# Optimization experiments

Measured on AMD Instinct MI355X. Metric: run time of the kernel, lower is better.

## Reference

```python
import jax, jax.numpy as jnp
import numpy as np

B, N, L, C, H = 2, 3000, 6, 128, 1
IN_DIM = 6
SIGMA_D = 1.0
EPS = 1e-5
DH = C // H


def _conv1(x, W, b):
    # pointwise Conv1d: x [B,Cin,N], W [Cout,Cin], b [Cout]
    return jnp.einsum('oc,bcn->bon', W, x) + b[None, :, None]


def _bn(x, g, beta):
    # BatchNorm1d (training-mode batch stats) over (B, N) per channel
    m = x.mean(axis=(0, 2), keepdims=True)
    v = x.var(axis=(0, 2), keepdims=True)
    return g[None, :, None] * (x - m) * jax.lax.rsqrt(v + EPS) + beta[None, :, None]


def setup_inputs() -> dict:
    key = jax.random.key(0)
    ks = iter(jax.random.split(key, 80))

    def w(shape, fan_in):
        return jax.random.normal(next(ks), shape, jnp.float32) * (1.0 / np.sqrt(fan_in))

    src = jax.random.normal(next(ks), (B, N, 3), jnp.float32)
    tgt = src + 0.1 * jax.random.normal(next(ks), (B, N, 3), jnp.float32)
    corr_pos = jnp.concatenate([src, tgt], axis=-1)  # [B,N,6]

    d = {
        'corr_pos': corr_pos, 'src_keypts': src, 'tgt_keypts': tgt,
        'init_W': w((C, IN_DIM), IN_DIM), 'init_b': jnp.zeros((C,), jnp.float32),
        'pcn_W': w((L, C, C), C), 'pcn_b': jnp.zeros((L, C), jnp.float32),
        'pcn_g': jnp.ones((L, C), jnp.float32), 'pcn_beta': jnp.zeros((L, C), jnp.float32),
        'qW': w((L, C, C), C), 'qb': jnp.zeros((L, C), jnp.float32),
        'kW': w((L, C, C), C), 'kb': jnp.zeros((L, C), jnp.float32),
        'vW': w((L, C, C), C), 'vb': jnp.zeros((L, C), jnp.float32),
        'm1W': w((L, C // 2, C), C), 'm1b': jnp.zeros((L, C // 2), jnp.float32),
        'm1g': jnp.ones((L, C // 2), jnp.float32), 'm1beta': jnp.zeros((L, C // 2), jnp.float32),
        'm2W': w((L, C // 2, C // 2), C // 2), 'm2b': jnp.zeros((L, C // 2), jnp.float32),
        'm2g': jnp.ones((L, C // 2), jnp.float32), 'm2beta': jnp.zeros((L, C // 2), jnp.float32),
        'm3W': w((L, C, C // 2), C // 2), 'm3b': jnp.zeros((L, C), jnp.float32),
        'c1W': w((32, C), C), 'c1b': jnp.zeros((32,), jnp.float32),
        'c2W': w((32, 32), 32), 'c2b': jnp.zeros((32,), jnp.float32),
        'c3W': w((1, 32), 32), 'c3b': jnp.zeros((1,), jnp.float32),
    }
    return d


def reference(corr_pos, src_keypts, tgt_keypts, init_W, init_b,
              pcn_W, pcn_b, pcn_g, pcn_beta,
              qW, qb, kW, kb, vW, vb,
              m1W, m1b, m1g, m1beta, m2W, m2b, m2g, m2beta, m3W, m3b,
              c1W, c1b, c2W, c2b, c3W, c3b):
    # spatial compatibility: clamp(1 - (d_src - d_tgt)^2 / sigma_d^2, min=0)  [B,N,N]
    src_dist = jnp.linalg.norm(src_keypts[:, :, None, :] - src_keypts[:, None, :, :], axis=-1)
    tgt_dist = jnp.linalg.norm(tgt_keypts[:, :, None, :] - tgt_keypts[:, None, :, :], axis=-1)
    sc = jnp.maximum(1.0 - (src_dist - tgt_dist) ** 2 / SIGMA_D ** 2, 0.0)

    # init embedding: [B,C,N]
    x = _conv1(jnp.swapaxes(corr_pos, 1, 2), init_W, init_b)
    scale = 1.0 / jnp.sqrt(jnp.float32(DH))

    for i in range(L):
        # PointCN layer
        x = jax.nn.relu(_bn(_conv1(x, pcn_W[i], pcn_b[i]), pcn_g[i], pcn_beta[i]))
        # NonLocal block
        Q = _conv1(x, qW[i], qb[i]).reshape(B, H, DH, N)
        K = _conv1(x, kW[i], kb[i]).reshape(B, H, DH, N)
        V = _conv1(x, vW[i], vb[i]).reshape(B, H, DH, N)
        scores = jnp.einsum('bhco,bhci->bhoi', Q, K) * scale  # [B,H,N,N]
        weight = jax.nn.softmax(sc[:, None, :, :] * scores, axis=-1)
        msg = jnp.einsum('bhoi,bhci->bhco', weight, V).reshape(B, C, N)
        msg = jax.nn.relu(_bn(_conv1(msg, m1W[i], m1b[i]), m1g[i], m1beta[i]))
        msg = jax.nn.relu(_bn(_conv1(msg, m2W[i], m2b[i]), m2g[i], m2beta[i]))
        msg = _conv1(msg, m3W[i], m3b[i])
        x = x + msg

    corr_feat = x
    norm = jnp.maximum(jnp.linalg.norm(corr_feat, axis=1, keepdims=True), 1e-12)
    normed_corr_feat = corr_feat / norm
    h = jax.nn.relu(_conv1(corr_feat, c1W, c1b))
    h = jax.nn.relu(_conv1(h, c2W, c2b))
    confidence = _conv1(h, c3W, c3b)[:, 0, :]  # [B,N]
    return confidence, normed_corr_feat
```

## Files before the change

kernel.cpp:

```cpp
#include <hip/hip_runtime.h>
#include <hip/hip_bf16.h>


#define BB 2
#define NN 3000
#define CC 128
#define LAYERS 6
#define BN_EPS 1e-5f
#define ATT_SCALE 0.08838834764831845f
#define INV_CNT (1.f / (float)(BB * NN))

typedef _Float16 f16;
typedef _Float16 f16x8 __attribute__((ext_vector_type(8)));
typedef float f32x4 __attribute__((ext_vector_type(4)));

__global__ void init_conv(const float* __restrict__ corr, const float* __restrict__ W,
                          const float* __restrict__ bias, float* __restrict__ x) {
  int idx = blockIdx.x * 256 + threadIdx.x;
  if (idx >= BB * CC * NN) return;
  int n = idx % NN;
  int c = (idx / NN) % CC;
  int b = idx / (NN * CC);
  const float* cp = corr + (b * NN + n) * 6;
  float acc = bias[c];
#pragma unroll
  for (int d = 0; d < 6; ++d) acc += W[c * 6 + d] * cp[d];
  x[idx] = acc;
}

template <int CIN, int COUT, int NP, int MODE, int CSPLIT, int BNIN, int STATS>
__launch_bounds__(256)
__global__ void conv_k(const float* __restrict__ in, float* __restrict__ out,
                       const float* __restrict__ W, const float* __restrict__ bias,
                       const float* __restrict__ res,
                       const float* __restrict__ isums, const float* __restrict__ ig,
                       const float* __restrict__ ibeta,
                       const float* __restrict__ rsums, const float* __restrict__ rg,
                       const float* __restrict__ rbeta, float* __restrict__ osums) {
  constexpr int COB = COUT / CSPLIT;
  constexpr int CH = (CIN > 64) ? 64 : CIN;
  constexpr int PG = NP / 4;
  constexpr int KPT = COB * PG / 256;
  constexpr int XROW = (NP == 16) ? 20 : 32;
  __shared__ alignas(16) float Xs[CIN][XROW];
  __shared__ float Ws[COB][CH + 1];
  __shared__ float bnsc[BNIN ? CIN : 1], bnsh[BNIN ? CIN : 1];
  const int tid = threadIdx.x;
  const int p0 = blockIdx.x * NP;
  const int co0 = blockIdx.y * COB;

  if (BNIN) {
    for (int c = tid; c < CIN; c += 256) {
      float s = isums[c], s2 = isums[CIN + c];
      float mean = s * INV_CNT;
      float var = s2 * INV_CNT - mean * mean;
      float sc = ig[c] * rsqrtf(var + BN_EPS);
      bnsc[c] = sc;
      bnsh[c] = ibeta[c] - mean * sc;
    }
    __syncthreads();
  }

  for (int idx = tid; idx < CIN * NP; idx += 256) {
    int ci = idx / NP, j = idx % NP;
    int p = p0 + j;
    float v = 0.f;
    if (p < BB * NN) {
      int b = p / NN, n = p % NN;
      v = in[(b * CIN + ci) * NN + n];
      if (BNIN) {
        v = v * bnsc[ci] + bnsh[ci];
        v = v > 0.f ? v : 0.f;
      }
    }
    Xs[ci][j] = v;
  }

  const int nb = (tid % PG) * 4;
  const int cb = (tid / PG) * KPT;

  float acc[KPT][4];
#pragma unroll
  for (int k = 0; k < KPT; ++k)
#pragma unroll
    for (int j = 0; j < 4; ++j) acc[k][j] = 0.f;

  for (int c0 = 0; c0 < CIN; c0 += CH) {
    __syncthreads();
    for (int idx = tid; idx < COB * CH; idx += 256) {
      int co = idx / CH, cc = idx % CH;
      Ws[co][cc] = W[(co0 + co) * CIN + c0 + cc];
    }
    __syncthreads();
#pragma unroll 4
    for (int cc = 0; cc < CH; ++cc) {
      float4 xv = *reinterpret_cast<const float4*>(&Xs[c0 + cc][nb]);
#pragma unroll
      for (int k = 0; k < KPT; ++k) {
        float w = Ws[cb + k][cc];
        acc[k][0] += w * xv.x;
        acc[k][1] += w * xv.y;
        acc[k][2] += w * xv.z;
        acc[k][3] += w * xv.w;
      }
    }
  }

#pragma unroll
  for (int k = 0; k < KPT; ++k) {
    int co = co0 + cb + k;
    float bv = bias[co];
    float rsc = 0.f, rsh = 0.f;
    if (MODE == 3) {
      float s = rsums[co], s2 = rsums[COUT + co];
      float mean = s * INV_CNT;
      float var = s2 * INV_CNT - mean * mean;
      rsc = rg[co] * rsqrtf(var + BN_EPS);
      rsh = rbeta[co] - mean * rsc;
    }
    float sp = 0.f, sp2 = 0.f;
#pragma unroll
    for (int j = 0; j < 4; ++j) {
      int p = p0 + nb + j;
      if (p < BB * NN) {
        int b = p / NN, n = p % NN;
        int o = (b * COUT + co) * NN + n;
        float v = acc[k][j] + bv;
        if (MODE == 3) {
          float rr = res[o] * rsc + rsh;
          v += (rr > 0.f ? rr : 0.f);
        }
        out[o] = v;
        if (STATS) {
          sp += v;
          sp2 += v * v;
        }
      }
    }
    if (STATS) {
#pragma unroll
      for (int d = 1; d < PG; d <<= 1) {
        sp += __shfl_xor(sp, d);
        sp2 += __shfl_xor(sp2, d);
      }
      if ((tid & (PG - 1)) == 0) {
        atomicAdd(&osums[co], sp);
        atomicAdd(&osums[COUT + co], sp2);
      }
    }
  }
}

__launch_bounds__(256)
__global__ void conv_qkv(const float* __restrict__ Yp, const float* __restrict__ psums,
                         const float* __restrict__ pg, const float* __restrict__ pbeta,
                         const float* __restrict__ qW, const float* __restrict__ kW,
                         const float* __restrict__ vW, const float* __restrict__ qb,
                         const float* __restrict__ kb, const float* __restrict__ vb,
                         f16* __restrict__ Qh, f16* __restrict__ Ql,
                         f16* __restrict__ Kh, f16* __restrict__ Kl,
                         f16* __restrict__ Vh, f16* __restrict__ Vl) {
  __shared__ alignas(16) float Xs[128][32];
  __shared__ float Ws[64][65];
  __shared__ float bnsc[128], bnsh[128];
  const int tid = threadIdx.x;
  const int p0 = blockIdx.x * 32;
  const int sel = blockIdx.y >> 1;
  const int co0 = (blockIdx.y & 1) * 64;
  const float* W = (sel == 0) ? qW : (sel == 1) ? kW : vW;
  const float* bias = (sel == 0) ? qb : (sel == 1) ? kb : vb;

  for (int c = tid; c < 128; c += 256) {
    float s = psums[c], s2 = psums[128 + c];
    float mean = s * INV_CNT;
    float var = s2 * INV_CNT - mean * mean;
    float sc = pg[c] * rsqrtf(var + BN_EPS);
    bnsc[c] = sc;
    bnsh[c] = pbeta[c] - mean * sc;
  }
  __syncthreads();

  for (int idx = tid; idx < 128 * 32; idx += 256) {
    int ci = idx >> 5, j = idx & 31;
    int p = p0 + j;
    float v = 0.f;
    if (p < BB * NN) {
      int b = p / NN, n = p % NN;
      v = Yp[(b * 128 + ci) * NN + n];
      v = v * bnsc[ci] + bnsh[ci];
      v = v > 0.f ? v : 0.f;
    }
    Xs[ci][j] = v;
  }

  const int nb = (tid % 8) * 4;
  const int cb = (tid / 8) * 2;
  float acc[2][4] = {{0.f, 0.f, 0.f, 0.f}, {0.f, 0.f, 0.f, 0.f}};

  for (int c0 = 0; c0 < 128; c0 += 64) {
    __syncthreads();
    for (int idx = tid; idx < 64 * 64; idx += 256) {
      int co = idx >> 6, cc = idx & 63;
      Ws[co][cc] = W[(co0 + co) * 128 + c0 + cc];
    }
    __syncthreads();
#pragma unroll 4
    for (int cc = 0; cc < 64; ++cc) {
      float4 xv = *reinterpret_cast<const float4*>(&Xs[c0 + cc][nb]);
#pragma unroll
      for (int k = 0; k < 2; ++k) {
        float w = Ws[cb + k][cc];
        acc[k][0] += w * xv.x;
        acc[k][1] += w * xv.y;
        acc[k][2] += w * xv.z;
        acc[k][3] += w * xv.w;
      }
    }
  }

#pragma unroll
  for (int k = 0; k < 2; ++k) {
    int co = co0 + cb + k;
    float bv = bias[co];
#pragma unroll
    for (int j = 0; j < 4; ++j) {
      int p = p0 + nb + j;
      if (p < BB * NN) {
        int b = p / NN, n = p % NN;
        float v = acc[k][j] + bv;
        f16 h = (f16)v;
        f16 lo = (f16)(v - (float)h);
        if (sel == 0) {
          size_t o = (size_t)(b * NN + n) * CC + co;
          Qh[o] = h; Ql[o] = lo;
        } else if (sel == 1) {
          size_t o = (size_t)(b * NN + n) * CC + co;
          Kh[o] = h; Kl[o] = lo;
        } else {
          size_t o = (size_t)(b * CC + co) * NN + n;
          Vh[o] = h; Vl[o] = lo;
        }
      }
    }
  }
}

__launch_bounds__(512)
__global__ void attn_mf7(const f16* __restrict__ Qhp, const f16* __restrict__ Qlp,
                         const f16* __restrict__ Khp, const f16* __restrict__ Klp,
                         const f16* __restrict__ Vhp, const f16* __restrict__ Vlp,
                         const float* __restrict__ srcp, const float* __restrict__ tgtp,
                         float* __restrict__ pacc, float* __restrict__ pm,
                         float* __restrict__ pl, int chunk) {
  const int b = blockIdx.z;
  const int q0 = blockIdx.x * 128;
  const int s = blockIdx.y;
  const int cs = s * chunk;
  const int ce = min(cs + chunk, NN);
  const int tid = threadIdx.x;
  const int w = tid >> 6, lane = tid & 63, quad = lane >> 4, l15 = lane & 15;

  __shared__ f16 Ksh[32][136], Ksl[32][136];
  __shared__ f16 Vsh[128][40], Vsl[128][40];
  __shared__ f16 Ps[8][16][40];
  __shared__ float kps[6][36];

  float qp[4][6];
  const int orow = q0 + w * 16;
#pragma unroll
  for (int r = 0; r < 4; ++r) {
    int o = orow + quad * 4 + r;
    if (o >= NN) o = NN - 1;
#pragma unroll
    for (int d = 0; d < 3; ++d) {
      qp[r][d] = srcp[(b * NN + o) * 3 + d];
      qp[r][3 + d] = tgtp[(b * NN + o) * 3 + d];
    }
  }
  f16x8 qh[4], ql[4];
  {
    int o = orow + l15;
    if (o >= NN) o = NN - 1;
    size_t base = (size_t)(b * NN + o) * CC + quad * 8;
#pragma unroll
    for (int cc = 0; cc < 4; ++cc) {
      qh[cc] = *reinterpret_cast<const f16x8*>(Qhp + base + cc * 32);
      ql[cc] = *reinterpret_cast<const f16x8*>(Qlp + base + cc * 32);
    }
  }

  float m[4], l[4];
#pragma unroll
  for (int r = 0; r < 4; ++r) {
    m[r] = -1e30f;
    l[r] = 0.f;
  }
  f32x4 acco[8];
#pragma unroll
  for (int t = 0; t < 8; ++t) acco[t] = (f32x4){0.f, 0.f, 0.f, 0.f};

  const int NT = (ce - cs + 31) >> 5;
  for (int it = 0; it < NT; ++it) {
    const int kk0 = cs + it * 32;
    __syncthreads();
    for (int t = tid; t < 1024; t += 512) {
      int plane = t >> 9, row = (t >> 4) & 31, cu = t & 15;
      int kr = kk0 + row;
      if (kr >= NN) kr = NN - 1;
      const f16* src = (plane ? Klp : Khp) + (size_t)(b * NN + kr) * CC + cu * 8;
      uint4 v = *reinterpret_cast<const uint4*>(src);
      f16* dst = plane ? &Ksl[row][cu * 8] : &Ksh[row][cu * 8];
      *reinterpret_cast<uint4*>(dst) = v;
    }
    for (int t = tid; t < 1024; t += 512) {
      int plane = t >> 9, c = (t >> 2) & 127, iu = t & 3;
      int kb = kk0 + iu * 8;
      if (kb > NN - 8) kb = NN - 8;
      const f16* src = (plane ? Vlp : Vhp) + (size_t)(b * CC + c) * NN + kb;
      uint4 v = *reinterpret_cast<const uint4*>(src);
      f16* dst = plane ? &Vsl[c][iu * 8] : &Vsh[c][iu * 8];
      *reinterpret_cast<uint4*>(dst) = v;
    }
    if (tid < 192) {
      int d = tid >> 5, i = tid & 31;
      int ig = kk0 + i;
      if (ig >= NN) ig = NN - 1;
      kps[d][i] = (d < 3) ? srcp[(b * NN + ig) * 3 + d] : tgtp[(b * NN + ig) * 3 + d - 3];
    }
    __syncthreads();

    f32x4 accs[2];
#pragma unroll
    for (int k4 = 0; k4 < 2; ++k4) accs[k4] = (f32x4){0.f, 0.f, 0.f, 0.f};
#pragma unroll
    for (int cc = 0; cc < 4; ++cc) {
#pragma unroll
      for (int k4 = 0; k4 < 2; ++k4) {
        f16x8 bh = *reinterpret_cast<const f16x8*>(&Ksh[k4 * 16 + l15][cc * 32 + quad * 8]);
        f16x8 bl = *reinterpret_cast<const f16x8*>(&Ksl[k4 * 16 + l15][cc * 32 + quad * 8]);
        accs[k4] = __builtin_amdgcn_mfma_f32_16x16x32_f16(qh[cc], bl, accs[k4], 0, 0, 0);
        accs[k4] = __builtin_amdgcn_mfma_f32_16x16x32_f16(ql[cc], bh, accs[k4], 0, 0, 0);
        accs[k4] = __builtin_amdgcn_mfma_f32_16x16x32_f16(qh[cc], bh, accs[k4], 0, 0, 0);
      }
    }

    float sv[2][4];
#pragma unroll
    for (int k4 = 0; k4 < 2; ++k4) {
      int iloc = k4 * 16 + l15;
      int ig = kk0 + iloc;
      float kx = kps[0][iloc], ky = kps[1][iloc], kz = kps[2][iloc];
      float tx = kps[3][iloc], ty = kps[4][iloc], tz = kps[5][iloc];
#pragma unroll
      for (int r = 0; r < 4; ++r) {
        float dx = qp[r][0] - kx, dy = qp[r][1] - ky, dz = qp[r][2] - kz;
        float ds2 = dx * dx + dy * dy + dz * dz;
        float ex = qp[r][3] - tx, ey = qp[r][4] - ty, ez = qp[r][5] - tz;
        float dt2 = ex * ex + ey * ey + ez * ez;
        float d2 = ds2 + dt2 - 2.f * sqrtf(ds2 * dt2);
        float gg = 1.f - d2;
        gg = gg > 0.f ? gg : 0.f;
        float val = accs[k4][r] * (ATT_SCALE * gg);
        sv[k4][r] = (ig < ce) ? val : -1e30f;
      }
    }

    float tmax[4];
#pragma unroll
    for (int r = 0; r < 4; ++r) tmax[r] = fmaxf(sv[0][r], sv[1][r]);
#pragma unroll
    for (int d = 1; d <= 8; d <<= 1)
#pragma unroll
      for (int r = 0; r < 4; ++r) tmax[r] = fmaxf(tmax[r], __shfl_xor(tmax[r], d));

    float alpha[4], ps[4];
    f16 pf[2][4];
#pragma unroll
    for (int r = 0; r < 4; ++r) {
      float mn = fmaxf(m[r], tmax[r]);
      alpha[r] = __expf(m[r] - mn);
      m[r] = mn;
      pf[0][r] = (f16)__expf(sv[0][r] - mn);
      pf[1][r] = (f16)__expf(sv[1][r] - mn);
      ps[r] = (float)pf[0][r] + (float)pf[1][r];
    }
#pragma unroll
    for (int d = 1; d <= 8; d <<= 1)
#pragma unroll
      for (int r = 0; r < 4; ++r) ps[r] += __shfl_xor(ps[r], d);
#pragma unroll
    for (int r = 0; r < 4; ++r) {
      l[r] = l[r] * alpha[r] + ps[r];
#pragma unroll
      for (int t = 0; t < 8; ++t) acco[t][r] *= alpha[r];
    }
#pragma unroll
    for (int r = 0; r < 4; ++r) {
      Ps[w][quad * 4 + r][l15] = pf[0][r];
      Ps[w][quad * 4 + r][16 + l15] = pf[1][r];
    }
    __syncthreads();

    {
      f16x8 af = *reinterpret_cast<const f16x8*>(&Ps[w][l15][quad * 8]);
#pragma unroll
      for (int t = 0; t < 8; ++t) {
        f16x8 vh = *reinterpret_cast<const f16x8*>(&Vsh[t * 16 + l15][quad * 8]);
        f16x8 vl = *reinterpret_cast<const f16x8*>(&Vsl[t * 16 + l15][quad * 8]);
        acco[t] = __builtin_amdgcn_mfma_f32_16x16x32_f16(af, vl, acco[t], 0, 0, 0);
        acco[t] = __builtin_amdgcn_mfma_f32_16x16x32_f16(af, vh, acco[t], 0, 0, 0);
      }
    }
  }

  const int pidx = s * BB + b;
  if (l15 == 0) {
#pragma unroll
    for (int r = 0; r < 4; ++r) {
      int o = orow + quad * 4 + r;
      if (o < NN) {
        pm[pidx * NN + o] = m[r];
        pl[pidx * NN + o] = l[r];
      }
    }
  }
#pragma unroll
  for (int r = 0; r < 4; ++r) {
    int o = orow + quad * 4 + r;
    if (o < NN) {
      size_t base2 = ((size_t)pidx * NN + o) * CC;
#pragma unroll
      for (int t = 0; t < 8; ++t) pacc[base2 + t * 16 + l15] = acco[t][r];
    }
  }
}

__launch_bounds__(256)
__global__ void conv_m1(const float* __restrict__ pacc, const float* __restrict__ pm,
                        const float* __restrict__ pl, float* __restrict__ out,
                        const float* __restrict__ W, const float* __restrict__ bias,
                        float* __restrict__ osums, int ksplit) {
  __shared__ alignas(16) float Xs[128][20];
  __shared__ float Ws[64][65];
  __shared__ float Es[16][17];
  __shared__ float Li[16];
  const int tid = threadIdx.x;
  const int p0 = blockIdx.x * 16;

  if (tid < 16) {
    int p = p0 + tid;
    float Lv = 1.f;
    if (p < BB * NN) {
      int b = p / NN, o = p % NN;
      float M = -1e30f;
      for (int s = 0; s < ksplit; ++s) M = fmaxf(M, pm[(s * BB + b) * NN + o]);
      Lv = 0.f;
      for (int s = 0; s < ksplit; ++s) {
        int pi = s * BB + b;
        float e = __expf(pm[pi * NN + o] - M);
        Es[tid][s] = e;
        Lv += pl[pi * NN + o] * e;
      }
    } else {
      for (int s = 0; s < ksplit; ++s) Es[tid][s] = 0.f;
    }
    Li[tid] = 1.f / Lv;
  }
  __syncthreads();

  for (int idx = tid; idx < 512; idx += 256) {
    int j = idx >> 5, c4 = (idx & 31) * 4;
    int p = p0 + j;
    float4 a = {0.f, 0.f, 0.f, 0.f};
    if (p < BB * NN) {
      int b = p / NN, o = p % NN;
      for (int s = 0; s < ksplit; ++s) {
        float e = Es[j][s];
        const float4 pv = *reinterpret_cast<const float4*>(
            &pacc[((size_t)(s * BB + b) * NN + o) * CC + c4]);
        a.x += pv.x * e;
        a.y += pv.y * e;
        a.z += pv.z * e;
        a.w += pv.w * e;
      }
      float inv = Li[j];
      a.x *= inv; a.y *= inv; a.z *= inv; a.w *= inv;
    }
    Xs[c4][j] = a.x;
    Xs[c4 + 1][j] = a.y;
    Xs[c4 + 2][j] = a.z;
    Xs[c4 + 3][j] = a.w;
  }

  const int nb = (tid & 3) * 4;
  const int co = tid >> 2;
  float acc[4] = {0.f, 0.f, 0.f, 0.f};

  for (int c0 = 0; c0 < 128; c0 += 64) {
    __syncthreads();
    for (int idx = tid; idx < 64 * 64; idx += 256) {
      int cr = idx >> 6, cc = idx & 63;
      Ws[cr][cc] = W[cr * 128 + c0 + cc];
    }
    __syncthreads();
#pragma unroll 4
    for (int cc = 0; cc < 64; ++cc) {
      float4 xv = *reinterpret_cast<const float4*>(&Xs[c0 + cc][nb]);
      float w = Ws[co][cc];
      acc[0] += w * xv.x;
      acc[1] += w * xv.y;
      acc[2] += w * xv.z;
      acc[3] += w * xv.w;
    }
  }

  {
    float bv = bias[co];
    float sp = 0.f, sp2 = 0.f;
#pragma unroll
    for (int j = 0; j < 4; ++j) {
      int p = p0 + nb + j;
      if (p < BB * NN) {
        int b = p / NN, n = p % NN;
        float v = acc[j] + bv;
        out[(b * 64 + co) * NN + n] = v;
        sp += v;
        sp2 += v * v;
      }
    }
    sp += __shfl_xor(sp, 1);
    sp2 += __shfl_xor(sp2, 1);
    sp += __shfl_xor(sp, 2);
    sp2 += __shfl_xor(sp2, 2);
    if ((tid & 3) == 0) {
      atomicAdd(&osums[co], sp);
      atomicAdd(&osums[64 + co], sp2);
    }
  }
}

__launch_bounds__(256)
__global__ void head_all(const float* __restrict__ Xg,
                         const float* __restrict__ c1W, const float* __restrict__ c1b,
                         const float* __restrict__ c2W, const float* __restrict__ c2b,
                         const float* __restrict__ c3W, const float* __restrict__ c3b,
                         float* __restrict__ out) {
  __shared__ float Xs[128][33];
  __shared__ float W1[32][129];
  __shared__ float W2[32][33];
  __shared__ float Hs[32][33], H2s[32][33];
  __shared__ float Inv[32];
  const int tid = threadIdx.x;
  const int p0 = blockIdx.x * 32;
  const int j = tid >> 3, sub = tid & 7;

  for (int idx = tid; idx < 128 * 32; idx += 256) {
    int ci = idx >> 5, jj = idx & 31;
    int p = p0 + jj;
    float v = 0.f;
    if (p < BB * NN) {
      int b = p / NN, n = p % NN;
      v = Xg[(b * 128 + ci) * NN + n];
    }
    Xs[ci][jj] = v;
  }
  for (int idx = tid; idx < 32 * 128; idx += 256) {
    W1[idx >> 7][idx & 127] = c1W[idx];
  }
  for (int idx = tid; idx < 32 * 32; idx += 256) {
    W2[idx >> 5][idx & 31] = c2W[idx];
  }
  __syncthreads();

  {
    float h1v[4];
#pragma unroll
    for (int k = 0; k < 4; ++k) h1v[k] = c1b[sub * 4 + k];
    for (int ci = 0; ci < 128; ++ci) {
      float xv = Xs[ci][j];
#pragma unroll
      for (int k = 0; k < 4; ++k) h1v[k] += W1[sub * 4 + k][ci] * xv;
    }
#pragma unroll
    for (int k = 0; k < 4; ++k) Hs[j][sub * 4 + k] = h1v[k] > 0.f ? h1v[k] : 0.f;
  }
  __syncthreads();
  {
    float h2v[4];
#pragma unroll
    for (int k = 0; k < 4; ++k) h2v[k] = c2b[sub * 4 + k];
#pragma unroll
    for (int cc = 0; cc < 32; ++cc) {
      float hv = Hs[j][cc];
#pragma unroll
      for (int k = 0; k < 4; ++k) h2v[k] += W2[sub * 4 + k][cc] * hv;
    }
#pragma unroll
    for (int k = 0; k < 4; ++k) H2s[j][sub * 4 + k] = h2v[k] > 0.f ? h2v[k] : 0.f;
  }
  __syncthreads();

  float ssp = 0.f;
#pragma unroll
  for (int k = 0; k < 16; ++k) {
    float v = Xs[sub + 8 * k][j];
    ssp += v * v;
  }
  ssp += __shfl_xor(ssp, 1);
  ssp += __shfl_xor(ssp, 2);
  ssp += __shfl_xor(ssp, 4);

  if (sub == 0) {
    int p = p0 + j;
    if (p < BB * NN) {
      float conf = c3b[0];
#pragma unroll
      for (int c = 0; c < 32; ++c) conf += c3W[c] * H2s[j][c];
      out[p] = conf;
    }
    float nrm = sqrtf(ssp);
    nrm = nrm > 1e-12f ? nrm : 1e-12f;
    Inv[j] = 1.f / nrm;
  }
  __syncthreads();

  for (int idx = tid; idx < 128 * 32; idx += 256) {
    int c = idx >> 5, jj = idx & 31;
    int p = p0 + jj;
    if (p < BB * NN) {
      int b = p / NN, n = p % NN;
      out[BB * NN + (b * 128 + c) * NN + n] = Xs[c][jj] * Inv[jj];
    }
  }
}

extern "C" void kernel_launch(void* const* d_in, const int* in_sizes, int n_in,
                              void* d_out, int out_size, void* d_ws, size_t ws_size,
                              hipStream_t stream) {
  const float* corr = (const float*)d_in[0];
  const float* srcp = (const float*)d_in[1];
  const float* tgtp = (const float*)d_in[2];
  const float* initW = (const float*)d_in[3];
  const float* initb = (const float*)d_in[4];
  const float* pcnW = (const float*)d_in[5];
  const float* pcnb = (const float*)d_in[6];
  const float* pcng = (const float*)d_in[7];
  const float* pcnbeta = (const float*)d_in[8];
  const float* qW = (const float*)d_in[9];
  const float* qb = (const float*)d_in[10];
  const float* kW = (const float*)d_in[11];
  const float* kb = (const float*)d_in[12];
  const float* vW = (const float*)d_in[13];
  const float* vb = (const float*)d_in[14];
  const float* m1W = (const float*)d_in[15];
  const float* m1b = (const float*)d_in[16];
  const float* m1g = (const float*)d_in[17];
  const float* m1beta = (const float*)d_in[18];
  const float* m2W = (const float*)d_in[19];
  const float* m2b = (const float*)d_in[20];
  const float* m2g = (const float*)d_in[21];
  const float* m2beta = (const float*)d_in[22];
  const float* m3W = (const float*)d_in[23];
  const float* m3b = (const float*)d_in[24];
  const float* c1W = (const float*)d_in[25];
  const float* c1b = (const float*)d_in[26];
  const float* c2W = (const float*)d_in[27];
  const float* c2b = (const float*)d_in[28];
  const float* c3W = (const float*)d_in[29];
  const float* c3b = (const float*)d_in[30];

  const int FEAT = BB * CC * NN;
  const int PLANE = FEAT / 2;
  float* ws = (float*)d_ws;
  float* X = ws;
  float* Y = X + FEAT;
  float* QhF = Y + FEAT;
  float* QlF = QhF + PLANE;
  float* KhF = QlF + PLANE;
  float* KlF = KhF + PLANE;
  float* VhF = KlF + PLANE;
  float* VlF = VhF + PLANE;
  float* SB = VlF + PLANE;
  float* pacc = SB + 3072;
  f16* Qh = (f16*)QhF;
  f16* Ql = (f16*)QlF;
  f16* Kh = (f16*)KhF;
  f16* Kl = (f16*)KlF;
  f16* Vh = (f16*)VhF;
  f16* Vl = (f16*)VlF;
  float* T1 = QhF;
  float* T2 = KhF;

  const size_t base_f = (size_t)(2 * FEAT + 6 * PLANE + 3072);
  const size_t per_f = (size_t)BB * NN * CC + 2 * (size_t)BB * NN;
  int ksplit = 16;
  while (ksplit > 1 && (base_f + (size_t)ksplit * per_f) * 4 > ws_size) ksplit >>= 1;
  const int chunk = (((NN + ksplit - 1) / ksplit) + 7) & ~7;
  float* pm = pacc + (size_t)ksplit * BB * NN * CC;
  float* pl = pm + (size_t)ksplit * BB * NN;

  dim3 blk(256);
  const int PT32 = (BB * NN + 31) / 32;
  const int PT16 = (BB * NN + 15) / 16;
  const int G_FEAT = (FEAT + 255) / 256;

  hipMemsetAsync(SB, 0, 3072 * sizeof(float), stream);
  init_conv<<<G_FEAT, blk, 0, stream>>>(corr, initW, initb, X);

  for (int i = 0; i < LAYERS; ++i) {
    float* pcnS = SB + i * 512;
    float* m1S = pcnS + 256;
    float* m2S = m1S + 128;
    conv_k<128, 128, 16, 0, 2, 0, 1><<<dim3(PT16, 2), blk, 0, stream>>>(
        X, Y, pcnW + i * 16384, pcnb + i * 128, nullptr,
        nullptr, nullptr, nullptr, nullptr, nullptr, nullptr, pcnS);
    conv_qkv<<<dim3(PT32, 6), blk, 0, stream>>>(
        Y, pcnS, pcng + i * 128, pcnbeta + i * 128, qW + i * 16384, kW + i * 16384,
        vW + i * 16384, qb + i * 128, kb + i * 128, vb + i * 128,
        Qh, Ql, Kh, Kl, Vh, Vl);
    attn_mf7<<<dim3((NN + 127) / 128, ksplit, BB), dim3(512), 0, stream>>>(
        Qh, Ql, Kh, Kl, Vh, Vl, srcp, tgtp, pacc, pm, pl, chunk);
    conv_m1<<<PT16, blk, 0, stream>>>(pacc, pm, pl, T1, m1W + i * 8192, m1b + i * 64,
                                      m1S, ksplit);
    conv_k<64, 64, 16, 0, 1, 1, 1><<<dim3(PT16, 1), blk, 0, stream>>>(
        T1, T2, m2W + i * 4096, m2b + i * 64, nullptr,
        m1S, m1g + i * 64, m1beta + i * 64, nullptr, nullptr, nullptr, m2S);
    conv_k<64, 128, 16, 3, 2, 1, 0><<<dim3(PT16, 2), blk, 0, stream>>>(
        T2, X, m3W + i * 8192, m3b + i * 128, Y,
        m2S, m2g + i * 64, m2beta + i * 64, pcnS, pcng + i * 128, pcnbeta + i * 128,
        nullptr);
  }

  head_all<<<PT32, blk, 0, stream>>>(X, c1W, c1b, c2W, c2b, c3W, c3b, (float*)d_out);
}
```

Measured before the change: 1.356 ms.

## Use split-fp16 MFMA for PointCN and QKV pointwise convolutions

Replaces the scalar FP32 FMA kernels for the PointCN conv and the fused Q/K/V projection with MFMA-based kernels. Inputs and weights are split into high and low fp16 halves, and three 16x16x32 MFMAs per tile approximate FP32 accuracy. Each block now covers all 128 output channels (one wave per 32 channels), which halves the number of grid slices and removes the repeated input loads. This costs extra conversion work and precision only near FP32, while the attention kernel likely still dominates total time.

```diff
diff --git a/kernel.cpp b/kernel.cpp
--- a/kernel.cpp
+++ b/kernel.cpp
@@ -26,6 +26,230 @@
 #pragma unroll
   for (int d = 0; d < 6; ++d) acc += W[c * 6 + d] * cp[d];
   x[idx] = acc;
+}
+
+__launch_bounds__(256)
+__global__ void conv_mfma_pcn(const float* __restrict__ Xg, float* __restrict__ Y,
+                              const float* __restrict__ W, const float* __restrict__ bias,
+                              float* __restrict__ osums) {
+  __shared__ f16 Xsh[32][136], Xsl[32][136];
+  __shared__ f16 Wsh[128][40], Wsl[128][40];
+  const int tid = threadIdx.x;
+  const int p0 = blockIdx.x * 32;
+  const int w = tid >> 6, lane = tid & 63, quad = lane >> 4, l15 = lane & 15;
+  const int co0 = w * 32;
+
+  for (int idx = tid; idx < 512; idx += 256) {
+    int ci = (idx >> 5) * 8, j = idx & 31;
+    int p = p0 + j;
+    if (p >= BB * NN) p = BB * NN - 1;
+    int b = p / NN, n = p % NN;
+    f16x8 hv, lv;
+#pragma unroll
+    for (int t = 0; t < 8; ++t) {
+      float v = Xg[(b * 128 + ci + t) * NN + n];
+      f16 h = (f16)v;
+      hv[t] = h;
+      lv[t] = (f16)(v - (float)h);
+    }
+    *reinterpret_cast<f16x8*>(&Xsh[j][ci]) = hv;
+    *reinterpret_cast<f16x8*>(&Xsl[j][ci]) = lv;
+  }
+
+  f32x4 acc[2][2];
+#pragma unroll
+  for (int ct = 0; ct < 2; ++ct)
+#pragma unroll
+    for (int pt = 0; pt < 2; ++pt) acc[ct][pt] = (f32x4){0.f, 0.f, 0.f, 0.f};
+
+  for (int kc = 0; kc < 4; ++kc) {
+    __syncthreads();
+    for (int idx = tid; idx < 512; idx += 256) {
+      int co = idx >> 2, ks = idx & 3;
+      const float* wp = W + co * 128 + kc * 32 + ks * 8;
+      float4 w0 = *reinterpret_cast<const float4*>(wp);
+      float4 w1 = *reinterpret_cast<const float4*>(wp + 4);
+      float wv[8] = {w0.x, w0.y, w0.z, w0.w, w1.x, w1.y, w1.z, w1.w};
+      f16x8 hv, lv;
+#pragma unroll
+      for (int t = 0; t < 8; ++t) {
+        f16 h = (f16)wv[t];
+        hv[t] = h;
+        lv[t] = (f16)(wv[t] - (float)h);
+      }
+      *reinterpret_cast<f16x8*>(&Wsh[co][ks * 8]) = hv;
+      *reinterpret_cast<f16x8*>(&Wsl[co][ks * 8]) = lv;
+    }
+    __syncthreads();
+#pragma unroll
+    for (int ct = 0; ct < 2; ++ct) {
+      f16x8 ah = *reinterpret_cast<const f16x8*>(&Wsh[co0 + ct * 16 + l15][quad * 8]);
+      f16x8 al = *reinterpret_cast<const f16x8*>(&Wsl[co0 + ct * 16 + l15][quad * 8]);
+#pragma unroll
+      for (int pt = 0; pt < 2; ++pt) {
+        f16x8 bh = *reinterpret_cast<const f16x8*>(&Xsh[pt * 16 + l15][kc * 32 + quad * 8]);
+        f16x8 bl = *reinterpret_cast<const f16x8*>(&Xsl[pt * 16 + l15][kc * 32 + quad * 8]);
+        acc[ct][pt] = __builtin_amdgcn_mfma_f32_16x16x32_f16(ah, bl, acc[ct][pt], 0, 0, 0);
+        acc[ct][pt] = __builtin_amdgcn_mfma_f32_16x16x32_f16(al, bh, acc[ct][pt], 0, 0, 0);
+        acc[ct][pt] = __builtin_amdgcn_mfma_f32_16x16x32_f16(ah, bh, acc[ct][pt], 0, 0, 0);
+      }
+    }
+  }
+
+  float sp[2][4] = {{0.f}}, sp2[2][4] = {{0.f}};
+#pragma unroll
+  for (int ct = 0; ct < 2; ++ct)
+#pragma unroll
+    for (int pt = 0; pt < 2; ++pt) {
+      int p = p0 + pt * 16 + l15;
+      if (p < BB * NN) {
+        int b = p / NN, n = p % NN;
+#pragma unroll
+        for (int r = 0; r < 4; ++r) {
+          int co = co0 + ct * 16 + quad * 4 + r;
+          float v = acc[ct][pt][r] + bias[co];
+          Y[(b * 128 + co) * NN + n] = v;
+          sp[ct][r] += v;
+          sp2[ct][r] += v * v;
+        }
+      }
+    }
+#pragma unroll
+  for (int ct = 0; ct < 2; ++ct)
+#pragma unroll
+    for (int r = 0; r < 4; ++r)
+#pragma unroll
+      for (int d = 1; d <= 8; d <<= 1) {
+        sp[ct][r] += __shfl_xor(sp[ct][r], d);
+        sp2[ct][r] += __shfl_xor(sp2[ct][r], d);
+      }
+  if (l15 == 0) {
+#pragma unroll
+    for (int ct = 0; ct < 2; ++ct)
+#pragma unroll
+      for (int r = 0; r < 4; ++r) {
+        int co = co0 + ct * 16 + quad * 4 + r;
+        atomicAdd(&osums[co], sp[ct][r]);
+        atomicAdd(&osums[128 + co], sp2[ct][r]);
+      }
+  }
+}
+
+__launch_bounds__(256)
+__global__ void conv_mfma_qkv(const float* __restrict__ Yp, const float* __restrict__ psums,
+                              const float* __restrict__ pg, const float* __restrict__ pbeta,
+                              const float* __restrict__ qW, const float* __restrict__ kW,
+                              const float* __restrict__ vW, const float* __restrict__ qb,
+                              const float* __restrict__ kb, const float* __restrict__ vb,
+                              f16* __restrict__ Qh, f16* __restrict__ Ql,
+                              f16* __restrict__ Kh, f16* __restrict__ Kl,
+                              f16* __restrict__ Vh, f16* __restrict__ Vl) {
+  __shared__ f16 Xsh[32][136], Xsl[32][136];
+  __shared__ f16 Wsh[128][40], Wsl[128][40];
+  __shared__ float bnsc[128], bnsh[128];
+  const int tid = threadIdx.x;
+  const int p0 = blockIdx.x * 32;
+  const int sel = blockIdx.y;
+  const int w = tid >> 6, lane = tid & 63, quad = lane >> 4, l15 = lane & 15;
+  const int co0 = w * 32;
+  const float* W = (sel == 0) ? qW : (sel == 1) ? kW : vW;
+  const float* bias = (sel == 0) ? qb : (sel == 1) ? kb : vb;
+
+  for (int c = tid; c < 128; c += 256) {
+    float s = psums[c], s2 = psums[128 + c];
+    float mean = s * INV_CNT;
+    float var = s2 * INV_CNT - mean * mean;
+    float sc = pg[c] * rsqrtf(var + BN_EPS);
+    bnsc[c] = sc;
+    bnsh[c] = pbeta[c] - mean * sc;
+  }
+  __syncthreads();
+
+  for (int idx = tid; idx < 512; idx += 256) {
+    int ci = (idx >> 5) * 8, j = idx & 31;
+    int p = p0 + j;
+    if (p >= BB * NN) p = BB * NN - 1;
+    int b = p / NN, n = p % NN;
+    f16x8 hv, lv;
+#pragma unroll
+    for (int t = 0; t < 8; ++t) {
+      float v = Yp[(b * 128 + ci + t) * NN + n];
+      v = v * bnsc[ci + t] + bnsh[ci + t];
+      v = v > 0.f ? v : 0.f;
+      f16 h = (f16)v;
+      hv[t] = h;
+      lv[t] = (f16)(v - (float)h);
+    }
+    *reinterpret_cast<f16x8*>(&Xsh[j][ci]) = hv;
+    *reinterpret_cast<f16x8*>(&Xsl[j][ci]) = lv;
+  }
+
+  f32x4 acc[2][2];
+#pragma unroll
+  for (int ct = 0; ct < 2; ++ct)
+#pragma unroll
+    for (int pt = 0; pt < 2; ++pt) acc[ct][pt] = (f32x4){0.f, 0.f, 0.f, 0.f};
+
+  for (int kc = 0; kc < 4; ++kc) {
+    __syncthreads();
+    for (int idx = tid; idx < 512; idx += 256) {
+      int co = idx >> 2, ks = idx & 3;
+      const float* wp = W + co * 128 + kc * 32 + ks * 8;
+      float4 w0 = *reinterpret_cast<const float4*>(wp);
+      float4 w1 = *reinterpret_cast<const float4*>(wp + 4);
+      float wv[8] = {w0.x, w0.y, w0.z, w0.w, w1.x, w1.y, w1.z, w1.w};
+      f16x8 hv, lv;
+#pragma unroll
+      for (int t = 0; t < 8; ++t) {
+        f16 h = (f16)wv[t];
+        hv[t] = h;
+        lv[t] = (f16)(wv[t] - (float)h);
+      }
+      *reinterpret_cast<f16x8*>(&Wsh[co][ks * 8]) = hv;
+      *reinterpret_cast<f16x8*>(&Wsl[co][ks * 8]) = lv;
+    }
+    __syncthreads();
+#pragma unroll
+    for (int ct = 0; ct < 2; ++ct) {
+      f16x8 ah = *reinterpret_cast<const f16x8*>(&Wsh[co0 + ct * 16 + l15][quad * 8]);
+      f16x8 al = *reinterpret_cast<const f16x8*>(&Wsl[co0 + ct * 16 + l15][quad * 8]);
+#pragma unroll
+      for (int pt = 0; pt < 2; ++pt) {
+        f16x8 bh = *reinterpret_cast<const f16x8*>(&Xsh[pt * 16 + l15][kc * 32 + quad * 8]);
+        f16x8 bl = *reinterpret_cast<const f16x8*>(&Xsl[pt * 16 + l15][kc * 32 + quad * 8]);
+        acc[ct][pt] = __builtin_amdgcn_mfma_f32_16x16x32_f16(ah, bl, acc[ct][pt], 0, 0, 0);
+        acc[ct][pt] = __builtin_amdgcn_mfma_f32_16x16x32_f16(al, bh, acc[ct][pt], 0, 0, 0);
+        acc[ct][pt] = __builtin_amdgcn_mfma_f32_16x16x32_f16(ah, bh, acc[ct][pt], 0, 0, 0);
+      }
+    }
+  }
+
+#pragma unroll
+  for (int ct = 0; ct < 2; ++ct)
+#pragma unroll
+    for (int pt = 0; pt < 2; ++pt) {
+      int p = p0 + pt * 16 + l15;
+      if (p < BB * NN) {
+        int b = p / NN, n = p % NN;
+#pragma unroll
+        for (int r = 0; r < 4; ++r) {
+          int co = co0 + ct * 16 + quad * 4 + r;
+          float v = acc[ct][pt][r] + bias[co];
+          f16 h = (f16)v;
+          f16 lo = (f16)(v - (float)h);
+          if (sel == 0) {
+            size_t o = (size_t)(b * NN + n) * CC + co;
+            Qh[o] = h; Ql[o] = lo;
+          } else if (sel == 1) {
+            size_t o = (size_t)(b * NN + n) * CC + co;
+            Kh[o] = h; Kl[o] = lo;
+          } else {
+            size_t o = (size_t)(b * CC + co) * NN + n;
+            Vh[o] = h; Vl[o] = lo;
+          }
+        }
+      }
+    }
 }
 
 template <int CIN, int COUT, int NP, int MODE, int CSPLIT, int BNIN, int STATS>
@@ -146,100 +370,6 @@
       if ((tid & (PG - 1)) == 0) {
         atomicAdd(&osums[co], sp);
         atomicAdd(&osums[COUT + co], sp2);
-      }
-    }
-  }
-}
-
-__launch_bounds__(256)
-__global__ void conv_qkv(const float* __restrict__ Yp, const float* __restrict__ psums,
-                         const float* __restrict__ pg, const float* __restrict__ pbeta,
-                         const float* __restrict__ qW, const float* __restrict__ kW,
-                         const float* __restrict__ vW, const float* __restrict__ qb,
-                         const float* __restrict__ kb, const float* __restrict__ vb,
-                         f16* __restrict__ Qh, f16* __restrict__ Ql,
-                         f16* __restrict__ Kh, f16* __restrict__ Kl,
-                         f16* __restrict__ Vh, f16* __restrict__ Vl) {
-  __shared__ alignas(16) float Xs[128][32];
-  __shared__ float Ws[64][65];
-  __shared__ float bnsc[128], bnsh[128];
-  const int tid = threadIdx.x;
-  const int p0 = blockIdx.x * 32;
-  const int sel = blockIdx.y >> 1;
-  const int co0 = (blockIdx.y & 1) * 64;
-  const float* W = (sel == 0) ? qW : (sel == 1) ? kW : vW;
-  const float* bias = (sel == 0) ? qb : (sel == 1) ? kb : vb;
-
-  for (int c = tid; c < 128; c += 256) {
-    float s = psums[c], s2 = psums[128 + c];
-    float mean = s * INV_CNT;
-    float var = s2 * INV_CNT - mean * mean;
-    float sc = pg[c] * rsqrtf(var + BN_EPS);
-    bnsc[c] = sc;
-    bnsh[c] = pbeta[c] - mean * sc;
-  }
-  __syncthreads();
-
-  for (int idx = tid; idx < 128 * 32; idx += 256) {
-    int ci = idx >> 5, j = idx & 31;
-    int p = p0 + j;
-    float v = 0.f;
-    if (p < BB * NN) {
-      int b = p / NN, n = p % NN;
-      v = Yp[(b * 128 + ci) * NN + n];
-      v = v * bnsc[ci] + bnsh[ci];
-      v = v > 0.f ? v : 0.f;
-    }
-    Xs[ci][j] = v;
-  }
-
-  const int nb = (tid % 8) * 4;
-  const int cb = (tid / 8) * 2;
-  float acc[2][4] = {{0.f, 0.f, 0.f, 0.f}, {0.f, 0.f, 0.f, 0.f}};
-
-  for (int c0 = 0; c0 < 128; c0 += 64) {
-    __syncthreads();
-    for (int idx = tid; idx < 64 * 64; idx += 256) {
-      int co = idx >> 6, cc = idx & 63;
-      Ws[co][cc] = W[(co0 + co) * 128 + c0 + cc];
-    }
-    __syncthreads();
-#pragma unroll 4
-    for (int cc = 0; cc < 64; ++cc) {
-      float4 xv = *reinterpret_cast<const float4*>(&Xs[c0 + cc][nb]);
-#pragma unroll
-      for (int k = 0; k < 2; ++k) {
-        float w = Ws[cb + k][cc];
-        acc[k][0] += w * xv.x;
-        acc[k][1] += w * xv.y;
-        acc[k][2] += w * xv.z;
-        acc[k][3] += w * xv.w;
-      }
-    }
-  }
-
-#pragma unroll
-  for (int k = 0; k < 2; ++k) {
-    int co = co0 + cb + k;
-    float bv = bias[co];
-#pragma unroll
-    for (int j = 0; j < 4; ++j) {
-      int p = p0 + nb + j;
-      if (p < BB * NN) {
-        int b = p / NN, n = p % NN;
-        float v = acc[k][j] + bv;
-        f16 h = (f16)v;
-        f16 lo = (f16)(v - (float)h);
-        if (sel == 0) {
-          size_t o = (size_t)(b * NN + n) * CC + co;
-          Qh[o] = h; Ql[o] = lo;
-        } else if (sel == 1) {
-          size_t o = (size_t)(b * NN + n) * CC + co;
-          Kh[o] = h; Kl[o] = lo;
-        } else {
-          size_t o = (size_t)(b * CC + co) * NN + n;
-          Vh[o] = h; Vl[o] = lo;
-        }
       }
     }
   }
@@ -711,10 +841,8 @@
     float* pcnS = SB + i * 512;
     float* m1S = pcnS + 256;
     float* m2S = m1S + 128;
-    conv_k<128, 128, 16, 0, 2, 0, 1><<<dim3(PT16, 2), blk, 0, stream>>>(
-        X, Y, pcnW + i * 16384, pcnb + i * 128, nullptr,
-        nullptr, nullptr, nullptr, nullptr, nullptr, nullptr, pcnS);
-    conv_qkv<<<dim3(PT32, 6), blk, 0, stream>>>(
+    conv_mfma_pcn<<<PT32, blk, 0, stream>>>(X, Y, pcnW + i * 16384, pcnb + i * 128, pcnS);
+    conv_mfma_qkv<<<dim3(PT32, 3), blk, 0, stream>>>(
         Y, pcnS, pcng + i * 128, pcnbeta + i * 128, qW + i * 16384, kW + i * 16384,
         vW + i * 16384, qb + i * 128, kb + i * 128, vb + i * 128,
         Qh, Ql, Kh, Kl, Vh, Vl);
```

After: 1.296 ms. 4.4% less time.
